# Performance work log

Measured on AMD Instinct MI355X. Metric: run time of the kernel, lower is better.

Reference implementation:

```python
import jax, jax.numpy as jnp
import numpy as np

# Hyperparameters from init_kwargs (DGALoss(w, min_N, max_N, dt, huber))
W = 1.0e6
MIN_N = 4
MAX_N = 5
DT = 0.01
HUBER = 0.005
N0 = 5
MIN_FREQ = 2 ** MIN_N  # 16


def _skew(v):
    # v: (..., 3) -> (..., 3, 3)
    x, y, z = v[..., 0], v[..., 1], v[..., 2]
    O = jnp.zeros_like(x)
    return jnp.stack([
        jnp.stack([O, -z, y], -1),
        jnp.stack([z, O, -x], -1),
        jnp.stack([-y, x, O], -1)], -2)


def so3_exp(phi):
    # Rodrigues formula, phi: (n, 3) -> (n, 3, 3)
    theta2 = jnp.sum(phi * phi, axis=-1, keepdims=True)  # (n, 1)
    small = theta2 < 1e-12
    theta2_safe = jnp.where(small, 1.0, theta2)
    theta = jnp.sqrt(theta2_safe)
    a = jnp.where(small, 1.0 - theta2 / 6.0, jnp.sin(theta) / theta)[..., None]
    b = jnp.where(small, 0.5 - theta2 / 24.0, (1.0 - jnp.cos(theta)) / theta2_safe)[..., None]
    K = _skew(phi)
    I = jnp.eye(3, dtype=phi.dtype)
    return I + a * K + b * jnp.einsum('nij,njk->nik', K, K)


def so3_log(R):
    # R: (n, 3, 3) -> (n, 3); clip keeps arccos/sin grad-safe, exact to ~1e-6
    tr = R[..., 0, 0] + R[..., 1, 1] + R[..., 2, 2]
    cos = jnp.clip(0.5 * (tr - 1.0), -1.0 + 1e-6, 1.0 - 1e-6)
    theta = jnp.arccos(cos)
    factor = theta / (2.0 * jnp.sin(theta))
    vee = jnp.stack([R[..., 2, 1] - R[..., 1, 2],
                     R[..., 0, 2] - R[..., 2, 0],
                     R[..., 1, 0] - R[..., 0, 1]], -1)
    return factor[..., None] * vee


def _bmm(a, b):
    return jnp.einsum('nij,njk->nik', a, b)


def _bmtm(a, b):
    # a^T @ b per batch element (torch bmtm)
    return jnp.einsum('nji,njk->nik', a, b)


def _smooth_l1(x):
    # torch.nn.SmoothL1Loss(beta=1) against zeros, mean reduction
    ax = jnp.abs(x)
    return jnp.mean(jnp.where(ax < 1.0, 0.5 * ax * ax, ax - 0.5))


def _f_huber(rs):
    return W * _smooth_l1(rs / HUBER) * HUBER ** 2


def _forward(xs, w_hat):
    N = xs.shape[0]
    # ground-truth increments at the coarsest level
    Xs = so3_exp(xs[:, ::MIN_FREQ].reshape(-1, 3))          # (N*T/16, 3, 3)
    Om = so3_exp((DT * w_hat).reshape(-1, 3))               # (N*T, 3, 3)
    # tree reduction: compose adjacent rotations min_N times
    for _ in range(MIN_N):
        Om = _bmm(Om[::2], Om[1::2])
    rs = so3_log(_bmtm(Om, Xs)).reshape(N, -1, 3)[:, N0:]
    loss = _f_huber(rs)
    for k in range(MIN_N, MAX_N):
        Om = _bmm(Om[::2], Om[1::2])
        Xs = _bmm(Xs[::2], Xs[1::2])
        rs = so3_log(_bmtm(Om, Xs)).reshape(N, -1, 3)[:, N0:]
        loss = loss + _f_huber(rs) / 2 ** (k - MIN_N + 1)
    return loss


def setup_inputs() -> dict:
    key = jax.random.key(0)
    k1, k2 = jax.random.split(key)
    # xs are ground-truth orientation increments over dt -> small rotations
    xs = 0.01 * jax.random.normal(k1, (64, 32768, 3), dtype=jnp.float32)
    w_hat = jax.random.normal(k2, (64, 32768, 3), dtype=jnp.float32)
    return {"xs": xs, "w_hat": w_hat}


def reference(xs, w_hat):
    return _forward(xs, w_hat)
```

## Files before the change

### kernel.cpp

```cpp
#include <hip/hip_runtime.h>
#include <math.h>


#define NB 512
#define NT 256

__device__ __forceinline__ float4 qmul(float4 a, float4 b) {
    return make_float4(
        a.x * b.x - a.y * b.y - a.z * b.z - a.w * b.w,
        a.x * b.y + a.y * b.x + a.z * b.w - a.w * b.z,
        a.x * b.z + a.z * b.x + a.w * b.y - a.y * b.w,
        a.x * b.w + a.w * b.x + a.y * b.z - a.z * b.y);
}

__device__ __forceinline__ float4 qconj(float4 a) {
    return make_float4(a.x, -a.y, -a.z, -a.w);
}

template <bool SCALE01>
__device__ __forceinline__ float4 qexp(float x, float y, float z) {
    float n2 = x * x + y * y + z * z;
    float t2 = SCALE01 ? 1e-4f * n2 : n2;
    float cw = 1.0f + t2 * (-0.125f + t2 * (1.0f / 384.0f));
    float k = 0.5f + t2 * (-1.0f / 48.0f + t2 * (1.0f / 3840.0f));
    if (SCALE01) k *= 0.01f;
    return make_float4(cw, k * x, k * y, k * z);
}

__device__ __forceinline__ float huber1(float v) {
    v = fabsf(v) * 200.0f;
    return v < 1.0f ? 0.5f * v * v : v - 0.5f;
}

__device__ __forceinline__ float log_huber_q(float4 r) {
    float vn2 = r.y * r.y + r.z * r.z + r.w * r.w;
    float c = 1.0f - 2.0f * vn2;
    c = fminf(fmaxf(c, -1.0f + 1e-6f), 1.0f - 1e-6f);
    float th = acosf(c);
    float s2 = (1.0f - c) * (1.0f + c);
    float fac = th * 0.5f * rsqrtf(s2);
    float k = fac * 4.0f * r.x;
    return huber1(k * r.y) + huber1(k * r.z) + huber1(k * r.w);
}

__global__ __launch_bounds__(NT) void dga_main_q(
        const float* __restrict__ xs, const float* __restrict__ wh,
        float* __restrict__ partial) {
    const int tid = blockIdx.x * NT + threadIdx.x;

    float buf[48];
    const float4* p = reinterpret_cast<const float4*>(wh + (size_t)tid * 48);
#pragma unroll
    for (int j = 0; j < 12; ++j)
        reinterpret_cast<float4*>(buf)[j] = p[j];

    float4 q = qexp<true>(buf[0], buf[1], buf[2]);
#pragma unroll
    for (int i = 1; i < 16; ++i)
        q = qmul(q, qexp<true>(buf[3 * i], buf[3 * i + 1], buf[3 * i + 2]));

    float4 xv = *reinterpret_cast<const float4*>(xs + (size_t)tid * 48);
    float4 xq = qexp<false>(xv.x, xv.y, xv.z);

    float s1 = 0.0f, s2 = 0.0f;
    if ((tid & 2047) >= 5)
        s1 = log_huber_q(qmul(qconj(q), xq));

    float4 qo, xo;
    qo.x = __shfl_xor(q.x, 1);  qo.y = __shfl_xor(q.y, 1);
    qo.z = __shfl_xor(q.z, 1);  qo.w = __shfl_xor(q.w, 1);
    xo.x = __shfl_xor(xq.x, 1); xo.y = __shfl_xor(xq.y, 1);
    xo.z = __shfl_xor(xq.z, 1); xo.w = __shfl_xor(xq.w, 1);
    if ((threadIdx.x & 1) == 0 && ((tid >> 1) & 1023) >= 5) {
        float4 q2 = qmul(q, qo);
        float4 x2 = qmul(xq, xo);
        s2 = log_huber_q(qmul(qconj(q2), x2));
    }

#pragma unroll
    for (int off = 32; off; off >>= 1) {
        s1 += __shfl_down(s1, off);
        s2 += __shfl_down(s2, off);
    }
    __shared__ float sh1[4], sh2[4];
    int lane = threadIdx.x & 63, wv = threadIdx.x >> 6;
    if (lane == 0) { sh1[wv] = s1; sh2[wv] = s2; }
    __syncthreads();
    if (threadIdx.x == 0) {
        partial[blockIdx.x]      = sh1[0] + sh1[1] + sh1[2] + sh1[3];
        partial[NB + blockIdx.x] = sh2[0] + sh2[1] + sh2[2] + sh2[3];
    }
}

__global__ __launch_bounds__(NT) void dga_final_q(
        const float* __restrict__ partial, float* __restrict__ out) {
    int t = threadIdx.x;
    double v1 = (double)partial[t] + (double)partial[t + 256];
    double v2 = (double)partial[NB + t] + (double)partial[NB + t + 256];
#pragma unroll
    for (int off = 32; off; off >>= 1) {
        v1 += __shfl_down(v1, off);
        v2 += __shfl_down(v2, off);
    }
    __shared__ double a1[4], a2[4];
    int lane = t & 63, wv = t >> 6;
    if (lane == 0) { a1[wv] = v1; a2[wv] = v2; }
    __syncthreads();
    if (t == 0) {
        double S1 = a1[0] + a1[1] + a1[2] + a1[3];
        double S2 = a2[0] + a2[1] + a2[2] + a2[3];
        out[0] = (float)(S1 * (25.0 / 392256.0) + S2 * (12.5 / 195648.0));
    }
}

extern "C" void kernel_launch(void* const* d_in, const int* in_sizes, int n_in,
                              void* d_out, int out_size, void* d_ws, size_t ws_size,
                              hipStream_t stream) {
    const float* xs = (const float*)d_in[0];
    const float* wh = (const float*)d_in[1];
    float* out = (float*)d_out;
    float* partial = (float*)d_ws;

    dga_main_q<<<NB, NT, 0, stream>>>(xs, wh, partial);
    dga_final_q<<<1, NT, 0, stream>>>(partial, out);
}
```

Measured before the change: 15.32 us.

## Split each 16-step composition across two threads and combine via shuffle

Each group of 16 angular-rate samples is now handled by two threads, each composing 8 quaternion exponentials, with the halves combined through a lane shuffle in the correct order. The grid doubles to 1024 blocks, the level-2 pairing moves to xor-2 shuffles, and the final reduction loops over the larger partial array. The goal is to shorten the serial qmul chain per thread and raise the number of waves in flight to hide load latency. The cost is extra shuffles, redundant xs loads, and half the threads sitting idle during the log/huber stage.

```diff
diff --git a/kernel.cpp b/kernel.cpp
--- a/kernel.cpp
+++ b/kernel.cpp
@@ -2,7 +2,7 @@
 #include <math.h>
 
 
-#define NB 512
+#define NB 1024
 #define NT 256
 
 __device__ __forceinline__ float4 qmul(float4 a, float4 b) {
@@ -43,37 +43,44 @@
     return huber1(k * r.y) + huber1(k * r.z) + huber1(k * r.w);
 }
 
+__device__ __forceinline__ float4 shflx(float4 v, int m) {
+    return make_float4(__shfl_xor(v.x, m), __shfl_xor(v.y, m),
+                       __shfl_xor(v.z, m), __shfl_xor(v.w, m));
+}
+
 __global__ __launch_bounds__(NT) void dga_main_q(
         const float* __restrict__ xs, const float* __restrict__ wh,
         float* __restrict__ partial) {
     const int tid = blockIdx.x * NT + threadIdx.x;
+    const int g = tid >> 1;
+    const int h = tid & 1;
 
-    float buf[48];
-    const float4* p = reinterpret_cast<const float4*>(wh + (size_t)tid * 48);
+    float buf[24];
+    const float4* p = reinterpret_cast<const float4*>(wh + (size_t)g * 48 + h * 24);
 #pragma unroll
-    for (int j = 0; j < 12; ++j)
+    for (int j = 0; j < 6; ++j)
         reinterpret_cast<float4*>(buf)[j] = p[j];
+    float4 xv = *reinterpret_cast<const float4*>(xs + (size_t)g * 48);
 
     float4 q = qexp<true>(buf[0], buf[1], buf[2]);
 #pragma unroll
-    for (int i = 1; i < 16; ++i)
+    for (int i = 1; i < 8; ++i)
         q = qmul(q, qexp<true>(buf[3 * i], buf[3 * i + 1], buf[3 * i + 2]));
 
-    float4 xv = *reinterpret_cast<const float4*>(xs + (size_t)tid * 48);
+    float4 qo = shflx(q, 1);
+    float4 qf = h ? qmul(qo, q) : qmul(q, qo);
+
     float4 xq = qexp<false>(xv.x, xv.y, xv.z);
 
     float s1 = 0.0f, s2 = 0.0f;
-    if ((tid & 2047) >= 5)
-        s1 = log_huber_q(qmul(qconj(q), xq));
+    if (h == 0 && (g & 2047) >= 5)
+        s1 = log_huber_q(qmul(qconj(qf), xq));
 
-    float4 qo, xo;
-    qo.x = __shfl_xor(q.x, 1);  qo.y = __shfl_xor(q.y, 1);
-    qo.z = __shfl_xor(q.z, 1);  qo.w = __shfl_xor(q.w, 1);
-    xo.x = __shfl_xor(xq.x, 1); xo.y = __shfl_xor(xq.y, 1);
-    xo.z = __shfl_xor(xq.z, 1); xo.w = __shfl_xor(xq.w, 1);
-    if ((threadIdx.x & 1) == 0 && ((tid >> 1) & 1023) >= 5) {
-        float4 q2 = qmul(q, qo);
-        float4 x2 = qmul(xq, xo);
+    float4 q2o = shflx(qf, 2);
+    float4 x2o = shflx(xq, 2);
+    if ((tid & 3) == 0 && ((g >> 1) & 1023) >= 5) {
+        float4 q2 = qmul(qf, q2o);
+        float4 x2 = qmul(xq, x2o);
         s2 = log_huber_q(qmul(qconj(q2), x2));
     }
 
@@ -95,8 +102,12 @@
 __global__ __launch_bounds__(NT) void dga_final_q(
         const float* __restrict__ partial, float* __restrict__ out) {
     int t = threadIdx.x;
-    double v1 = (double)partial[t] + (double)partial[t + 256];
-    double v2 = (double)partial[NB + t] + (double)partial[NB + t + 256];
+    double v1 = 0.0, v2 = 0.0;
+#pragma unroll
+    for (int j = 0; j < NB / 256; ++j) {
+        v1 += (double)partial[t + 256 * j];
+        v2 += (double)partial[NB + t + 256 * j];
+    }
 #pragma unroll
     for (int off = 32; off; off >>= 1) {
         v1 += __shfl_down(v1, off);
```

Result: faster. 15.01 us (-2.0%).
